# Kernel optimization log

Hardware: AMD Instinct MI355X
Metric: run time of the kernel (lower is better)

Reference implementation:

```python
import jax, jax.numpy as jnp
import numpy as np

B, T, F, H = 128, 1024, 256, 512  # batch, seq_len (input_dims[0]), features (input_dims[1]), rnn_size


def _lstm(xWb, U, reverse=False, return_sequences=False):
    """Keras-semantics LSTM. xWb: [B,T,4H] = x @ W + b precomputed. Gate order i,f,g,o."""
    Hn = U.shape[0]
    xs = jnp.swapaxes(xWb, 0, 1)  # [T,B,4H] for scan over time
    h0 = jnp.zeros((xWb.shape[0], Hn), xWb.dtype)
    c0 = h0

    def step(carry, xw):
        h, c = carry
        z = xw + h @ U  # [B,4H]
        i, f, g, o = jnp.split(z, 4, axis=-1)
        i = jax.nn.sigmoid(i)
        f = jax.nn.sigmoid(f)
        g = jnp.tanh(g)
        o = jax.nn.sigmoid(o)
        c = f * c + i * g
        h = o * jnp.tanh(c)
        return (h, c), h

    (hT, _), hs = jax.lax.scan(step, (h0, c0), xs, reverse=reverse)
    if return_sequences:
        return jnp.swapaxes(hs, 0, 1)  # [B,T,H]
    return hT  # [B,H] final state (for reverse=True this is the state after t=0)


def setup_inputs() -> dict:
    key = jax.random.key(0)
    ks = jax.random.split(key, 9)
    g = lambda k, shape: (jax.random.normal(k, shape, jnp.float32) * 0.05)
    return {
        "x": jax.random.uniform(ks[0], (B, T, F), jnp.float32),
        # encoder forward-direction LSTM
        "Wf": g(ks[1], (F, 4 * H)), "Uf": g(ks[2], (H, 4 * H)), "bf": jnp.zeros((4 * H,), jnp.float32),
        # encoder backward-direction LSTM
        "Wb": g(ks[3], (F, 4 * H)), "Ub": g(ks[4], (H, 4 * H)), "bb": jnp.zeros((4 * H,), jnp.float32),
        # decoder LSTM (input is concat latent, 2H wide)
        "Wd": g(ks[5], (2 * H, 4 * H)), "Ud": g(ks[6], (H, 4 * H)), "bd": jnp.zeros((4 * H,), jnp.float32),
        # TimeDistributed Dense
        "Wo": g(ks[7], (H, F)), "bo": jnp.zeros((F,), jnp.float32),
    }


def reference(x, Wf, Uf, bf, Wb, Ub, bb, Wd, Ud, bd, Wo, bo):
    # Encoder: Bidirectional(LSTM(H)) -> concat final states [B, 2H]
    h_fwd = _lstm(x @ Wf + bf, Uf, reverse=False)
    h_bwd = _lstm(x @ Wb + bb, Ub, reverse=True)
    latent = jnp.concatenate([h_fwd, h_bwd], axis=-1)  # [B, 2H]
    # Decoder: RepeatVector(T) -> LSTM(H, return_sequences) -> TimeDistributed(Dense(F))
    rep = jnp.broadcast_to(latent[:, None, :], (x.shape[0], x.shape[1], 2 * H))  # [B,T,2H]
    dec = _lstm(rep @ Wd + bd, Ud, return_sequences=True)  # [B,T,H]
    return dec @ Wo + bo  # [B,T,F]
```

## Files before the change

### kernel.cpp

```cpp
#include <hip/hip_runtime.h>
#include <stdint.h>

typedef unsigned short u16;
typedef short bf16x8 __attribute__((ext_vector_type(8)));
typedef float f32x4  __attribute__((ext_vector_type(4)));
typedef unsigned short u16x8 __attribute__((ext_vector_type(8)));
typedef unsigned int   u32x4 __attribute__((ext_vector_type(4)));

__device__ __forceinline__ u16 f2bf(float f) {
  uint32_t u = __float_as_uint(f);
  return (u16)((u + 0x7FFFu + ((u >> 16) & 1u)) >> 16);
}
__device__ __forceinline__ u16 f2bf6(float f) {
  uint32_t u = __float_as_uint(f);
  return (u16)(((u + 0xFFFFu + ((u >> 17) & 1u)) >> 17) << 1);
}
__device__ __forceinline__ float fsig(float x) {
  x = fminf(fmaxf(x, -30.f), 30.f);
  return __builtin_amdgcn_rcpf(1.f + __builtin_amdgcn_exp2f(-1.44269504088896f * x));
}
__device__ __forceinline__ float ftanhf(float x) {
  x = fminf(fmaxf(x, -10.f), 10.f);
  float e = __builtin_amdgcn_exp2f(2.88539008177793f * x);
  return (e - 1.f) * __builtin_amdgcn_rcpf(e + 1.f);
}

__device__ __forceinline__ int flag_load(const int* p) {
  int v;
  asm volatile("global_load_dword %0, %1, off sc0 sc1\n\ts_waitcnt vmcnt(0)"
               : "=&v"(v) : "v"(p) : "memory");
  return v;
}
__device__ __forceinline__ void flag_store(int* p, int v) {
  asm volatile("global_store_dword %0, %1, off sc0 sc1" :: "v"(p), "v"(v) : "memory");
}
__device__ __forceinline__ void ld_chunk4(const u16* p, u32x4& a, u32x4& b,
                                          u32x4& c, u32x4& d) {
  asm volatile("global_load_dwordx4 %0, %4, off sc0 sc1\n\t"
               "global_load_dwordx4 %1, %4, off offset:16 sc0 sc1\n\t"
               "global_load_dwordx4 %2, %4, off offset:32 sc0 sc1\n\t"
               "global_load_dwordx4 %3, %4, off offset:48 sc0 sc1\n\t"
               "s_waitcnt vmcnt(0)"
               : "=&v"(a), "=&v"(b), "=&v"(c), "=&v"(d)
               : "v"(p) : "memory");
}
__device__ __forceinline__ void st_coh_x4(u16* p, u32x4 v) {
  asm volatile("global_store_dwordx4 %0, %1, off sc0 sc1" :: "v"(p), "v"(v) : "memory");
}
__device__ __forceinline__ uint4 ld_x4(const float* p) {
  uint4 v;
  asm volatile("global_load_dwordx4 %0, %1, off" : "=&v"(v) : "v"(p) : "memory");
  return v;
}
__device__ __forceinline__ void wait_vm0() {
  asm volatile("s_waitcnt vmcnt(0)" ::: "memory");
}
__device__ __forceinline__ bf16x8 pin_frag(const u16* p) {
  u32x4 v;
  asm volatile("global_load_dwordx4 %0, %1, off" : "=&v"(v) : "v"(p));
  return __builtin_bit_cast(bf16x8, v);
}
__device__ __forceinline__ uint32_t nib_of(u32x4 d) {
  return (d[0] & 1u) | ((d[1] & 1u) << 1) | ((d[2] & 1u) << 2) | ((d[3] & 1u) << 3);
}

__global__ void prep_kernel(const float* __restrict__ Wf, const float* __restrict__ Uf, const float* __restrict__ bf,
                            const float* __restrict__ Wb, const float* __restrict__ Ub, const float* __restrict__ bb,
                            const float* __restrict__ Wd, const float* __restrict__ Ud, const float* __restrict__ bd,
                            const float* __restrict__ Wo,
                            u16* __restrict__ encF, u16* __restrict__ encB,
                            u16* __restrict__ udF, u16* __restrict__ wdF, u16* __restrict__ woF,
                            float* __restrict__ biasF, float* __restrict__ biasB, float* __restrict__ biasD,
                            int* __restrict__ flagsAll, u16* __restrict__ hbE, u16* __restrict__ hbD)
{
  constexpr int NC_ENC = 128 * 24 * 64;
  constexpr int NC_UD  = 128 * 16 * 64;
  constexpr int NC_WD  = 128 * 32 * 64;
  constexpr int NC_WO  = 16 * 16 * 64;
  constexpr int B1 = 2 * NC_ENC;
  constexpr int B2 = B1 + NC_UD;
  constexpr int B3 = B2 + NC_WD;
  constexpr int B4 = B3 + NC_WO;
  constexpr int B5 = B4 + 768;
  constexpr int B6 = B5 + 64;
  constexpr int B7 = B6 + 32768;
  constexpr int TOTAL = B7 + 16384;

  for (int idx = blockIdx.x * 256 + threadIdx.x; idx < TOTAL; idx += gridDim.x * 256) {
    if (idx < B1) {
      int d = idx / NC_ENC;
      int r = idx - d * NC_ENC;
      int ntg = r / 1536;
      int rem = r - ntg * 1536;
      int kt = rem >> 6, lane = rem & 63;
      int np = ntg * 16 + (lane & 15);
      int col = (np & 3) * 512 + (np >> 2);
      int kb = kt * 32 + (lane >> 4) * 8;
      const float* W = d ? Wb : Wf;
      const float* U = d ? Ub : Uf;
      u16* dst = (d ? encB : encF) + (size_t)r * 8;
      if (kb < 256) {
        const float* s = W + (size_t)kb * 2048 + col;
#pragma unroll
        for (int e = 0; e < 8; ++e) dst[e] = f2bf(s[(size_t)e * 2048]);
      } else {
        const float* s = U + (size_t)(kb - 256) * 2048 + col;
#pragma unroll
        for (int e = 0; e < 8; ++e) dst[e] = f2bf(s[(size_t)e * 2048]);
      }
    } else if (idx < B2) {
      int r = idx - B1;
      int ntg = r / 1024;
      int rem = r - ntg * 1024;
      int kt = rem >> 6, lane = rem & 63;
      int np = ntg * 16 + (lane & 15);
      int col = (np & 3) * 512 + (np >> 2);
      int kb = kt * 32 + (lane >> 4) * 8;
      const float* s = Ud + (size_t)kb * 2048 + col;
      u16* dst = udF + (size_t)r * 8;
#pragma unroll
      for (int e = 0; e < 8; ++e) dst[e] = f2bf(s[(size_t)e * 2048]);
    } else if (idx < B3) {
      int r = idx - B2;
      int ntg = r / 2048;
      int rem = r - ntg * 2048;
      int kt = rem >> 6, lane = rem & 63;
      int np = ntg * 16 + (lane & 15);
      int col = (np & 3) * 512 + (np >> 2);
      int kb = kt * 32 + (lane >> 4) * 8;
      const float* s = Wd + (size_t)kb * 2048 + col;
      u16* dst = wdF + (size_t)r * 8;
#pragma unroll
      for (int e = 0; e < 8; ++e) dst[e] = f2bf(s[(size_t)e * 2048]);
    } else if (idx < B4) {
      int r = idx - B3;
      int nt = r / 1024;
      int rem = r - nt * 1024;
      int kt = rem >> 6, lane = rem & 63;
      int col = nt * 16 + (lane & 15);
      int kb = kt * 32 + (lane >> 4) * 8;
      const float* s = Wo + (size_t)kb * 256 + col;
      u16* dst = woF + (size_t)r * 8;
#pragma unroll
      for (int e = 0; e < 8; ++e) dst[e] = f2bf(s[(size_t)e * 256]);
    } else if (idx < B5) {
      int r = idx - B4;
      int which = r >> 8;
      int j0 = (r & 255) * 8;
      const float* src = (which == 0) ? bf : (which == 1) ? bb : bd;
      float* dstb = (which == 0) ? biasF : (which == 1) ? biasB : biasD;
#pragma unroll
      for (int e = 0; e < 8; ++e) {
        int np = j0 + e;
        dstb[np] = src[(np & 3) * 512 + (np >> 2)];
      }
    } else if (idx < B6) {
      int r = idx - B5;
#pragma unroll
      for (int e = 0; e < 8; ++e) flagsAll[r * 8 + e] = 0;
    } else if (idx < B7) {
      int r = idx - B6;
      u16x8 z = {0, 0, 0, 0, 0, 0, 0, 0};
      *(u16x8*)&hbE[(size_t)r * 8] = z;
    } else {
      int r = idx - B7;
      u16x8 z = {0, 0, 0, 0, 0, 0, 0, 0};
      *(u16x8*)&hbD[(size_t)r * 8] = z;
    }
  }
}


__global__ __launch_bounds__(256, 1) void enc_kernel(
    const float* __restrict__ x,
    const u16* __restrict__ encF, const u16* __restrict__ encB,
    const float* __restrict__ biasF, const float* __restrict__ biasB,
    float* __restrict__ latent, u16* __restrict__ hbuf, int* __restrict__ flags)
{
  const int bid = blockIdx.x;
  const int g   = bid & 15;
  const int wgi = bid >> 4;
  const int dir = g >> 3;
  const int rowBase = (g & 7) * 16;
  const int tid = threadIdx.x;
  const int lane = tid & 63;
  const int wave = tid >> 6;
  const int l15 = lane & 15;
  const int lk  = lane >> 4;

  __shared__ __attribute__((aligned(16))) u16   xlds[2][16][264];
  __shared__ __attribute__((aligned(16))) u16   Alds[16][520];
  __shared__ __attribute__((aligned(16))) float zlds[4][2][16][20];
  __shared__ __attribute__((aligned(16))) u16   hlds[4][16][8];

  const u16* wsrc = dir ? encB : encF;
  bf16x8 Breg[2][24];
#pragma unroll
  for (int n = 0; n < 2; ++n) {
    const int ntg = wgi * 8 + wave * 2 + n;
    const u16* fb = wsrc + (size_t)(ntg * 1536 + lane) * 8;
#pragma unroll
    for (int kt = 0; kt < 24; ++kt)
      Breg[n][kt] = pin_frag(fb + kt * 512);
  }
  wait_vm0();
  __builtin_amdgcn_sched_barrier(0);

  const float* bias = dir ? biasB : biasF;
  float bias_r[2];
  bias_r[0] = bias[(wgi * 8 + wave * 2 + 0) * 16 + l15];
  bias_r[1] = bias[(wgi * 8 + wave * 2 + 1) * 16 + l15];

  u16* myH = hbuf + (size_t)g * 16384;
  int* myFlags = flags + g * 16;
  const int xr = tid >> 4, xc = tid & 15;
  const int cb = tid >> 2;
  const int cr0 = (tid & 3) * 4;

  {
    const int t0 = dir ? 1023 : 0;
    const float* xp = x + ((size_t)(rowBase + xr) * 1024 + t0) * 256 + xc * 16;
    float4 f0 = *(const float4*)xp;
    float4 f1 = *(const float4*)(xp + 4);
    float4 f2 = *(const float4*)(xp + 8);
    float4 f3 = *(const float4*)(xp + 12);
    u16x8 a, b;
    a[0]=f2bf(f0.x); a[1]=f2bf(f0.y); a[2]=f2bf(f0.z); a[3]=f2bf(f0.w);
    a[4]=f2bf(f1.x); a[5]=f2bf(f1.y); a[6]=f2bf(f1.z); a[7]=f2bf(f1.w);
    b[0]=f2bf(f2.x); b[1]=f2bf(f2.y); b[2]=f2bf(f2.z); b[3]=f2bf(f2.w);
    b[4]=f2bf(f3.x); b[5]=f2bf(f3.y); b[6]=f2bf(f3.z); b[7]=f2bf(f3.w);
    *(u16x8*)&xlds[0][xr][xc * 16] = a;
    *(u16x8*)&xlds[0][xr][xc * 16 + 8] = b;
  }
  __syncthreads();

  float cc0 = 0.f, cc1 = 0.f;

  for (int s = 0; s < 1024; ++s) {
    f32x4 acc0 = {bias_r[0], bias_r[0], bias_r[0], bias_r[0]};
    f32x4 acc1 = {bias_r[1], bias_r[1], bias_r[1], bias_r[1]};
#pragma unroll
    for (int kt = 0; kt < 8; ++kt) {
      bf16x8 av = *(const bf16x8*)&xlds[s & 1][l15][kt * 32 + lk * 8];
      acc0 = __builtin_amdgcn_mfma_f32_16x16x32_bf16(av, Breg[0][kt], acc0, 0, 0, 0);
      acc1 = __builtin_amdgcn_mfma_f32_16x16x32_bf16(av, Breg[1][kt], acc1, 0, 0, 0);
    }

    const int sn = (s + 1 < 1024) ? s + 1 : 1023;
    const int tn = dir ? (1023 - sn) : sn;
    const float* xp = x + ((size_t)(rowBase + xr) * 1024 + tn) * 256 + xc * 16;
    uint4 xq0 = ld_x4(xp);
    uint4 xq1 = ld_x4(xp + 4);
    uint4 xq2 = ld_x4(xp + 8);
    uint4 xq3 = ld_x4(xp + 12);

    if (s > 0) {
      const uint32_t Texp = 8u | ((uint32_t)s & 7u);
      const u16* hs = myH + ((s - 1) & 1) * 8192 + cb * 128 + cr0 * 8;
      const int* pf = &myFlags[tid >> 4];
      u32x4 h0, h1, h2, h3;
      int it = 0;
      while (true) {
        ld_chunk4(hs, h0, h1, h2, h3);
        if (nib_of(h0) == Texp && nib_of(h1) == Texp &&
            nib_of(h2) == Texp && nib_of(h3) == Texp) break;
        if ((it & 3) == 3 && flag_load(pf) >= s) {
          ld_chunk4(hs, h0, h1, h2, h3);
          break;
        }
        __builtin_amdgcn_s_sleep(1);
        if (++it > 200000) break;
      }
      h0 &= ~1u; h1 &= ~1u; h2 &= ~1u; h3 &= ~1u;
      *(u32x4*)&Alds[cr0][cb * 8]     = h0;
      *(u32x4*)&Alds[cr0 + 1][cb * 8] = h1;
      *(u32x4*)&Alds[cr0 + 2][cb * 8] = h2;
      *(u32x4*)&Alds[cr0 + 3][cb * 8] = h3;
      __syncthreads();
#pragma unroll
      for (int kt = 0; kt < 16; ++kt) {
        bf16x8 av = *(const bf16x8*)&Alds[l15][kt * 32 + lk * 8];
        acc0 = __builtin_amdgcn_mfma_f32_16x16x32_bf16(av, Breg[0][kt + 8], acc0, 0, 0, 0);
        acc1 = __builtin_amdgcn_mfma_f32_16x16x32_bf16(av, Breg[1][kt + 8], acc1, 0, 0, 0);
      }
    } else {
      wait_vm0();
      __builtin_amdgcn_sched_barrier(0);
    }

#pragma unroll
    for (int r = 0; r < 4; ++r) {
      zlds[wave][0][lk * 4 + r][l15] = acc0[r];
      zlds[wave][1][lk * 4 + r][l15] = acc1[r];
    }
    asm volatile("s_waitcnt lgkmcnt(0)" ::: "memory");
    float4 g0 = *(const float4*)&zlds[wave][0][l15][lk * 4];
    float4 g1 = *(const float4*)&zlds[wave][1][l15][lk * 4];
    float hv0, hv1;
    { float iv = fsig(g0.x), fv = fsig(g0.y), gg = ftanhf(g0.z), ov = fsig(g0.w);
      cc0 = fv * cc0 + iv * gg;  hv0 = ov * ftanhf(cc0); }
    { float iv = fsig(g1.x), fv = fsig(g1.y), gg = ftanhf(g1.z), ov = fsig(g1.w);
      cc1 = fv * cc1 + iv * gg;  hv1 = ov * ftanhf(cc1); }

    if (s < 1023) {
      const uint32_t T = 8u | ((uint32_t)(s + 1) & 7u);
      u16 v0, v1;
      if ((lk & 1) == 0) {
        uint32_t b0 = (lk == 0) ? (T & 1u) : ((T >> 1) & 1u);
        uint32_t b1 = (lk == 0) ? ((T >> 2) & 1u) : ((T >> 3) & 1u);
        v0 = f2bf6(hv0) | (u16)b0;
        v1 = f2bf6(hv1) | (u16)b1;
      } else {
        v0 = f2bf(hv0);
        v1 = f2bf(hv1);
      }
      hlds[wave][l15][lk]     = v0;
      hlds[wave][l15][lk + 4] = v1;
      asm volatile("s_waitcnt lgkmcnt(0)" ::: "memory");
      if (lane < 16) {
        const u32x4 c = *(const u32x4*)&hlds[wave][lane][0];
        u16* hw = myH + (s & 1) * 8192 + (wgi * 4 + wave) * 128 + lane * 8;
        st_coh_x4(hw, c);
      }
    } else {
      float* lp = latent + (size_t)(rowBase + l15) * 1024 + dir * 512 + wgi * 32 + wave * 8 + lk;
      lp[0] = hv0;
      lp[4] = hv1;
    }

    {
      float4 f0 = __builtin_bit_cast(float4, xq0);
      float4 f1 = __builtin_bit_cast(float4, xq1);
      float4 f2 = __builtin_bit_cast(float4, xq2);
      float4 f3 = __builtin_bit_cast(float4, xq3);
      u16x8 a, b;
      a[0]=f2bf(f0.x); a[1]=f2bf(f0.y); a[2]=f2bf(f0.z); a[3]=f2bf(f0.w);
      a[4]=f2bf(f1.x); a[5]=f2bf(f1.y); a[6]=f2bf(f1.z); a[7]=f2bf(f1.w);
      b[0]=f2bf(f2.x); b[1]=f2bf(f2.y); b[2]=f2bf(f2.z); b[3]=f2bf(f2.w);
      b[4]=f2bf(f3.x); b[5]=f2bf(f3.y); b[6]=f2bf(f3.z); b[7]=f2bf(f3.w);
      *(u16x8*)&xlds[(s + 1) & 1][xr][xc * 16] = a;
      *(u16x8*)&xlds[(s + 1) & 1][xr][xc * 16 + 8] = b;
    }

    wait_vm0();
    __syncthreads();
    if (tid == 0 && s < 1023) flag_store(&myFlags[wgi], s + 1);
  }
}

__global__ __launch_bounds__(256, 1) void dec_kernel(
    const float* __restrict__ latent,
    const u16* __restrict__ udF, const u16* __restrict__ wdF, const u16* __restrict__ woF,
    const float* __restrict__ biasD, const float* __restrict__ bo,
    float* __restrict__ out, u16* __restrict__ hbuf, int* __restrict__ flags)
{
  const int bid = blockIdx.x;
  const int g   = bid & 7;
  const int wgi = bid >> 3;
  const int rowBase = g * 16;
  const int tid = threadIdx.x;
  const int lane = tid & 63;
  const int wave = tid >> 6;
  const int l15 = lane & 15;
  const int lk  = lane >> 4;

  __shared__ __attribute__((aligned(16))) u16   Llds[16][1032];
  __shared__ __attribute__((aligned(16))) u16   Alds[2][16][520];
  __shared__ __attribute__((aligned(16))) float zlds[4][2][16][20];
  __shared__ __attribute__((aligned(16))) u16   hlds[4][16][8];

#pragma unroll
  for (int c8 = 0; c8 < 8; ++c8) {
    const int idx = tid + c8 * 256;
    const int rr = idx >> 7, cf = idx & 127;
    const float* lp = latent + (size_t)(rowBase + rr) * 1024 + cf * 8;
    float4 v0 = *(const float4*)lp;
    float4 v1 = *(const float4*)(lp + 4);
    u16x8 tv;
    tv[0]=f2bf(v0.x); tv[1]=f2bf(v0.y); tv[2]=f2bf(v0.z); tv[3]=f2bf(v0.w);
    tv[4]=f2bf(v1.x); tv[5]=f2bf(v1.y); tv[6]=f2bf(v1.z); tv[7]=f2bf(v1.w);
    *(u16x8*)&Llds[rr][cf * 8] = tv;
  }
  __syncthreads();

  f32x4 xwd[2];
#pragma unroll
  for (int n = 0; n < 2; ++n) {
    const int ntg = wgi * 8 + wave * 2 + n;
    const float br = biasD[ntg * 16 + l15];
    f32x4 xw = {br, br, br, br};
    const u16* wf = wdF + (size_t)(ntg * 2048 + lane) * 8;
#pragma unroll
    for (int kt = 0; kt < 32; ++kt) {
      bf16x8 b = *(const bf16x8*)(wf + kt * 512);
      bf16x8 a = *(const bf16x8*)&Llds[l15][kt * 32 + lk * 8];
      xw = __builtin_amdgcn_mfma_f32_16x16x32_bf16(a, b, xw, 0, 0, 0);
    }
    xwd[n] = xw;
  }

  bf16x8 Bu[2][16];
#pragma unroll
  for (int n = 0; n < 2; ++n) {
    const int ntg = wgi * 8 + wave * 2 + n;
    const u16* ub = udF + (size_t)(ntg * 1024 + lane) * 8;
#pragma unroll
    for (int kt = 0; kt < 16; ++kt)
      Bu[n][kt] = pin_frag(ub + kt * 512);
  }
  bf16x8 Bo[16];
  if (wave == 0) {
    const u16* ob = woF + (size_t)(wgi * 1024 + lane) * 8;
#pragma unroll
    for (int kt = 0; kt < 16; ++kt)
      Bo[kt] = pin_frag(ob + kt * 512);
  }
  wait_vm0();
  __builtin_amdgcn_sched_barrier(0);
  const float bo_r = bo[wgi * 16 + l15];

  u16* myH = hbuf + (size_t)g * 16384;
  int* myFlags = flags + g * 16;
  const int cb = tid >> 2;
  const int cr0 = (tid & 3) * 4;

  float cc0 = 0.f, cc1 = 0.f;

  for (int t = 0; t < 1024; ++t) {
    f32x4 acc0 = xwd[0], acc1 = xwd[1];

    if (t > 0) {
      const uint32_t Texp = 8u | ((uint32_t)t & 7u);
      const u16* hs = myH + ((t - 1) & 1) * 8192 + cb * 128 + cr0 * 8;
      const int* pf = &myFlags[tid >> 4];
      u32x4 h0, h1, h2, h3;
      int it = 0;
      while (true) {
        ld_chunk4(hs, h0, h1, h2, h3);
        if (nib_of(h0) == Texp && nib_of(h1) == Texp &&
            nib_of(h2) == Texp && nib_of(h3) == Texp) break;
        if ((it & 3) == 3 && flag_load(pf) >= t) {
          ld_chunk4(hs, h0, h1, h2, h3);
          break;
        }
        __builtin_amdgcn_s_sleep(1);
        if (++it > 200000) break;
      }
      h0 &= ~1u; h1 &= ~1u; h2 &= ~1u; h3 &= ~1u;
      *(u32x4*)&Alds[t & 1][cr0][cb * 8]     = h0;
      *(u32x4*)&Alds[t & 1][cr0 + 1][cb * 8] = h1;
      *(u32x4*)&Alds[t & 1][cr0 + 2][cb * 8] = h2;
      *(u32x4*)&Alds[t & 1][cr0 + 3][cb * 8] = h3;
      __syncthreads();
#pragma unroll
      for (int kt = 0; kt < 16; ++kt) {
        bf16x8 av = *(const bf16x8*)&Alds[t & 1][l15][kt * 32 + lk * 8];
        acc0 = __builtin_amdgcn_mfma_f32_16x16x32_bf16(av, Bu[0][kt], acc0, 0, 0, 0);
        acc1 = __builtin_amdgcn_mfma_f32_16x16x32_bf16(av, Bu[1][kt], acc1, 0, 0, 0);
      }
    }

#pragma unroll
    for (int r = 0; r < 4; ++r) {
      zlds[wave][0][lk * 4 + r][l15] = acc0[r];
      zlds[wave][1][lk * 4 + r][l15] = acc1[r];
    }
    asm volatile("s_waitcnt lgkmcnt(0)" ::: "memory");
    float4 g0 = *(const float4*)&zlds[wave][0][l15][lk * 4];
    float4 g1 = *(const float4*)&zlds[wave][1][l15][lk * 4];
    float hv0, hv1;
    { float iv = fsig(g0.x), fv = fsig(g0.y), gg = ftanhf(g0.z), ov = fsig(g0.w);
      cc0 = fv * cc0 + iv * gg;  hv0 = ov * ftanhf(cc0); }
    { float iv = fsig(g1.x), fv = fsig(g1.y), gg = ftanhf(g1.z), ov = fsig(g1.w);
      cc1 = fv * cc1 + iv * gg;  hv1 = ov * ftanhf(cc1); }

    {
      const uint32_t T = 8u | ((uint32_t)(t + 1) & 7u);
      u16 v0, v1;
      if ((lk & 1) == 0) {
        uint32_t b0 = (lk == 0) ? (T & 1u) : ((T >> 1) & 1u);
        uint32_t b1 = (lk == 0) ? ((T >> 2) & 1u) : ((T >> 3) & 1u);
        v0 = f2bf6(hv0) | (u16)b0;
        v1 = f2bf6(hv1) | (u16)b1;
      } else {
        v0 = f2bf(hv0);
        v1 = f2bf(hv1);
      }
      hlds[wave][l15][lk]     = v0;
      hlds[wave][l15][lk + 4] = v1;
      asm volatile("s_waitcnt lgkmcnt(0)" ::: "memory");
      if (lane < 16) {
        const u32x4 c = *(const u32x4*)&hlds[wave][lane][0];
        u16* hw = myH + (t & 1) * 8192 + (wgi * 4 + wave) * 128 + lane * 8;
        st_coh_x4(hw, c);
      }
      wait_vm0();
      __syncthreads();
      if (tid == 0) flag_store(&myFlags[wgi], t + 1);
    }

    if (t > 0 && wave == 0) {
      f32x4 od = {bo_r, bo_r, bo_r, bo_r};
#pragma unroll
      for (int kt = 0; kt < 16; ++kt) {
        bf16x8 a = *(const bf16x8*)&Alds[t & 1][l15][kt * 32 + lk * 8];
        od = __builtin_amdgcn_mfma_f32_16x16x32_bf16(a, Bo[kt], od, 0, 0, 0);
      }
#pragma unroll
      for (int r = 0; r < 4; ++r)
        out[((size_t)(rowBase + lk * 4 + r) * 1024 + (t - 1)) * 256 + wgi * 16 + l15] = od[r];
    }
  }

  {
    const uint32_t Texp = 8u;
    const u16* hs = myH + 8192 + cb * 128 + cr0 * 8;
    const int* pf = &myFlags[tid >> 4];
    u32x4 h0, h1, h2, h3;
    int it = 0;
    while (true) {
      ld_chunk4(hs, h0, h1, h2, h3);
      if (nib_of(h0) == Texp && nib_of(h1) == Texp &&
          nib_of(h2) == Texp && nib_of(h3) == Texp) break;
      if ((it & 3) == 3 && flag_load(pf) >= 1024) {
        ld_chunk4(hs, h0, h1, h2, h3);
        break;
      }
      __builtin_amdgcn_s_sleep(1);
      if (++it > 200000) break;
    }
    h0 &= ~1u; h1 &= ~1u; h2 &= ~1u; h3 &= ~1u;
    *(u32x4*)&Alds[0][cr0][cb * 8]     = h0;
    *(u32x4*)&Alds[0][cr0 + 1][cb * 8] = h1;
    *(u32x4*)&Alds[0][cr0 + 2][cb * 8] = h2;
    *(u32x4*)&Alds[0][cr0 + 3][cb * 8] = h3;
    __syncthreads();
    if (wave == 0) {
      f32x4 od = {bo_r, bo_r, bo_r, bo_r};
#pragma unroll
      for (int kt = 0; kt < 16; ++kt) {
        bf16x8 a = *(const bf16x8*)&Alds[0][l15][kt * 32 + lk * 8];
        od = __builtin_amdgcn_mfma_f32_16x16x32_bf16(a, Bo[kt], od, 0, 0, 0);
      }
#pragma unroll
      for (int r = 0; r < 4; ++r)
        out[((size_t)(rowBase + lk * 4 + r) * 1024 + 1023) * 256 + wgi * 16 + l15] = od[r];
    }
  }
}

extern "C" void kernel_launch(void* const* d_in, const int* in_sizes, int n_in,
                              void* d_out, int out_size, void* d_ws, size_t ws_size,
                              hipStream_t stream)
{
  const float* x  = (const float*)d_in[0];
  const float* Wf = (const float*)d_in[1];
  const float* Uf = (const float*)d_in[2];
  const float* bf = (const float*)d_in[3];
  const float* Wb = (const float*)d_in[4];
  const float* Ub = (const float*)d_in[5];
  const float* bb = (const float*)d_in[6];
  const float* Wd = (const float*)d_in[7];
  const float* Ud = (const float*)d_in[8];
  const float* bd = (const float*)d_in[9];
  const float* Wo = (const float*)d_in[10];
  const float* bo = (const float*)d_in[11];

  if (ws_size < 14182400) return;

  char* ws = (char*)d_ws;
  u16*  encF   = (u16*)(ws + 0);
  u16*  encB   = (u16*)(ws + 3145728);
  u16*  udF    = (u16*)(ws + 6291456);
  u16*  wdF    = (u16*)(ws + 8388608);
  u16*  woF    = (u16*)(ws + 12582912);
  float* biasF = (float*)(ws + 12845056);
  float* biasB = (float*)(ws + 12853248);
  float* biasD = (float*)(ws + 12861440);
  float* latent= (float*)(ws + 12869632);
  u16*  hbufE  = (u16*)(ws + 13393920);
  u16*  hbufD  = (u16*)(ws + 13918208);
  int*  flagsE = (int*)(ws + 14180352);
  int*  flagsD = (int*)(ws + 14181376);

  prep_kernel<<<256, 256, 0, stream>>>(Wf, Uf, bf, Wb, Ub, bb, Wd, Ud, bd, Wo,
                                       encF, encB, udF, wdF, woF,
                                       biasF, biasB, biasD, flagsE, hbufE, hbufD);
  enc_kernel<<<256, 256, 0, stream>>>(x, encF, encB, biasF, biasB, latent, hbufE, flagsE);
  dec_kernel<<<128, 256, 0, stream>>>(latent, udF, wdF, woF, biasD, bo,
                                      (float*)d_out, hbufD, flagsD);
}
```

Baseline: 4.731 ms.

## Drop flag-based fallback sync and double-buffer recurrent h tile in LDS

Removes the per-step flag store/load handshake (and the wait_vm0 + extra barrier before it) from both encoder and decoder, relying solely on the tag bits embedded in the bf16 h values for cross-workgroup readiness. The encoder's recurrent A tile is now double-buffered in LDS so the h-load, x conversion and a single __syncthreads are merged before the recurrent MFMAs, eliminating one barrier per step. This shortens the serial per-timestep critical path, but it gives up the fallback path: if tagged stores become visible only partially, readers spin until the larger timeout.

```diff
diff --git a/kernel.cpp b/kernel.cpp
--- a/kernel.cpp
+++ b/kernel.cpp
@@ -25,15 +25,6 @@
   return (e - 1.f) * __builtin_amdgcn_rcpf(e + 1.f);
 }
 
-__device__ __forceinline__ int flag_load(const int* p) {
-  int v;
-  asm volatile("global_load_dword %0, %1, off sc0 sc1\n\ts_waitcnt vmcnt(0)"
-               : "=&v"(v) : "v"(p) : "memory");
-  return v;
-}
-__device__ __forceinline__ void flag_store(int* p, int v) {
-  asm volatile("global_store_dword %0, %1, off sc0 sc1" :: "v"(p), "v"(v) : "memory");
-}
 __device__ __forceinline__ void ld_chunk4(const u16* p, u32x4& a, u32x4& b,
                                           u32x4& c, u32x4& d) {
   asm volatile("global_load_dwordx4 %0, %4, off sc0 sc1\n\t"
@@ -175,7 +166,7 @@
     const float* __restrict__ x,
     const u16* __restrict__ encF, const u16* __restrict__ encB,
     const float* __restrict__ biasF, const float* __restrict__ biasB,
-    float* __restrict__ latent, u16* __restrict__ hbuf, int* __restrict__ flags)
+    float* __restrict__ latent, u16* __restrict__ hbuf)
 {
   const int bid = blockIdx.x;
   const int g   = bid & 15;
@@ -189,7 +180,7 @@
   const int lk  = lane >> 4;
 
   __shared__ __attribute__((aligned(16))) u16   xlds[2][16][264];
-  __shared__ __attribute__((aligned(16))) u16   Alds[16][520];
+  __shared__ __attribute__((aligned(16))) u16   Alds[2][16][520];
   __shared__ __attribute__((aligned(16))) float zlds[4][2][16][20];
   __shared__ __attribute__((aligned(16))) u16   hlds[4][16][8];
 
@@ -212,7 +203,6 @@
   bias_r[1] = bias[(wgi * 8 + wave * 2 + 1) * 16 + l15];
 
   u16* myH = hbuf + (size_t)g * 16384;
-  int* myFlags = flags + g * 16;
   const int xr = tid >> 4, xc = tid & 15;
   const int cb = tid >> 2;
   const int cr0 = (tid & 3) * 4;
@@ -257,77 +247,24 @@
     if (s > 0) {
       const uint32_t Texp = 8u | ((uint32_t)s & 7u);
       const u16* hs = myH + ((s - 1) & 1) * 8192 + cb * 128 + cr0 * 8;
-      const int* pf = &myFlags[tid >> 4];
       u32x4 h0, h1, h2, h3;
       int it = 0;
       while (true) {
         ld_chunk4(hs, h0, h1, h2, h3);
         if (nib_of(h0) == Texp && nib_of(h1) == Texp &&
             nib_of(h2) == Texp && nib_of(h3) == Texp) break;
-        if ((it & 3) == 3 && flag_load(pf) >= s) {
-          ld_chunk4(hs, h0, h1, h2, h3);
-          break;
-        }
         __builtin_amdgcn_s_sleep(1);
-        if (++it > 200000) break;
+        if (++it > 400000) break;
       }
       h0 &= ~1u; h1 &= ~1u; h2 &= ~1u; h3 &= ~1u;
-      *(u32x4*)&Alds[cr0][cb * 8]     = h0;
-      *(u32x4*)&Alds[cr0 + 1][cb * 8] = h1;
-      *(u32x4*)&Alds[cr0 + 2][cb * 8] = h2;
-      *(u32x4*)&Alds[cr0 + 3][cb * 8] = h3;
-      __syncthreads();
-#pragma unroll
-      for (int kt = 0; kt < 16; ++kt) {
-        bf16x8 av = *(const bf16x8*)&Alds[l15][kt * 32 + lk * 8];
-        acc0 = __builtin_amdgcn_mfma_f32_16x16x32_bf16(av, Breg[0][kt + 8], acc0, 0, 0, 0);
-        acc1 = __builtin_amdgcn_mfma_f32_16x16x32_bf16(av, Breg[1][kt + 8], acc1, 0, 0, 0);
-      }
+      *(u32x4*)&Alds[s & 1][cr0][cb * 8]     = h0;
+      *(u32x4*)&Alds[s & 1][cr0 + 1][cb * 8] = h1;
+      *(u32x4*)&Alds[s & 1][cr0 + 2][cb * 8] = h2;
+      *(u32x4*)&Alds[s & 1][cr0 + 3][cb * 8] = h3;
     } else {
       wait_vm0();
       __builtin_amdgcn_sched_barrier(0);
     }
-
-#pragma unroll
-    for (int r = 0; r < 4; ++r) {
-      zlds[wave][0][lk * 4 + r][l15] = acc0[r];
-      zlds[wave][1][lk * 4 + r][l15] = acc1[r];
-    }
-    asm volatile("s_waitcnt lgkmcnt(0)" ::: "memory");
-    float4 g0 = *(const float4*)&zlds[wave][0][l15][lk * 4];
-    float4 g1 = *(const float4*)&zlds[wave][1][l15][lk * 4];
-    float hv0, hv1;
-    { float iv = fsig(g0.x), fv = fsig(g0.y), gg = ftanhf(g0.z), ov = fsig(g0.w);
-      cc0 = fv * cc0 + iv * gg;  hv0 = ov * ftanhf(cc0); }
-    { float iv = fsig(g1.x), fv = fsig(g1.y), gg = ftanhf(g1.z), ov = fsig(g1.w);
-      cc1 = fv * cc1 + iv * gg;  hv1 = ov * ftanhf(cc1); }
-
-    if (s < 1023) {
-      const uint32_t T = 8u | ((uint32_t)(s + 1) & 7u);
-      u16 v0, v1;
-      if ((lk & 1) == 0) {
-        uint32_t b0 = (lk == 0) ? (T & 1u) : ((T >> 1) & 1u);
-        uint32_t b1 = (lk == 0) ? ((T >> 2) & 1u) : ((T >> 3) & 1u);
-        v0 = f2bf6(hv0) | (u16)b0;
-        v1 = f2bf6(hv1) | (u16)b1;
-      } else {
-        v0 = f2bf(hv0);
-        v1 = f2bf(hv1);
-      }
-      hlds[wave][l15][lk]     = v0;
-      hlds[wave][l15][lk + 4] = v1;
-      asm volatile("s_waitcnt lgkmcnt(0)" ::: "memory");
-      if (lane < 16) {
-        const u32x4 c = *(const u32x4*)&hlds[wave][lane][0];
-        u16* hw = myH + (s & 1) * 8192 + (wgi * 4 + wave) * 128 + lane * 8;
-        st_coh_x4(hw, c);
-      }
-    } else {
-      float* lp = latent + (size_t)(rowBase + l15) * 1024 + dir * 512 + wgi * 32 + wave * 8 + lk;
-      lp[0] = hv0;
-      lp[4] = hv1;
-    }
-
     {
       float4 f0 = __builtin_bit_cast(float4, xq0);
       float4 f1 = __builtin_bit_cast(float4, xq1);
@@ -341,10 +278,56 @@
       *(u16x8*)&xlds[(s + 1) & 1][xr][xc * 16] = a;
       *(u16x8*)&xlds[(s + 1) & 1][xr][xc * 16 + 8] = b;
     }
-
-    wait_vm0();
     __syncthreads();
-    if (tid == 0 && s < 1023) flag_store(&myFlags[wgi], s + 1);
+
+    if (s > 0) {
+#pragma unroll
+      for (int kt = 0; kt < 16; ++kt) {
+        bf16x8 av = *(const bf16x8*)&Alds[s & 1][l15][kt * 32 + lk * 8];
+        acc0 = __builtin_amdgcn_mfma_f32_16x16x32_bf16(av, Breg[0][kt + 8], acc0, 0, 0, 0);
+        acc1 = __builtin_amdgcn_mfma_f32_16x16x32_bf16(av, Breg[1][kt + 8], acc1, 0, 0, 0);
+      }
+    }
+
+#pragma unroll
+    for (int r = 0; r < 4; ++r) {
+      zlds[wave][0][lk * 4 + r][l15] = acc0[r];
+      zlds[wave][1][lk * 4 + r][l15] = acc1[r];
+    }
+    asm volatile("s_waitcnt lgkmcnt(0)" ::: "memory");
+    float4 g0 = *(const float4*)&zlds[wave][0][l15][lk * 4];
+    float4 g1 = *(const float4*)&zlds[wave][1][l15][lk * 4];
+    float hv0, hv1;
+    { float iv = fsig(g0.x), fv = fsig(g0.y), gg = ftanhf(g0.z), ov = fsig(g0.w);
+      cc0 = fv * cc0 + iv * gg;  hv0 = ov * ftanhf(cc0); }
+    { float iv = fsig(g1.x), fv = fsig(g1.y), gg = ftanhf(g1.z), ov = fsig(g1.w);
+      cc1 = fv * cc1 + iv * gg;  hv1 = ov * ftanhf(cc1); }
+
+    if (s < 1023) {
+      const uint32_t T = 8u | ((uint32_t)(s + 1) & 7u);
+      u16 v0, v1;
+      if ((lk & 1) == 0) {
+        uint32_t b0 = (lk == 0) ? (T & 1u) : ((T >> 1) & 1u);
+        uint32_t b1 = (lk == 0) ? ((T >> 2) & 1u) : ((T >> 3) & 1u);
+        v0 = f2bf6(hv0) | (u16)b0;
+        v1 = f2bf6(hv1) | (u16)b1;
+      } else {
+        v0 = f2bf(hv0);
+        v1 = f2bf(hv1);
+      }
+      hlds[wave][l15][lk]     = v0;
+      hlds[wave][l15][lk + 4] = v1;
+      asm volatile("s_waitcnt lgkmcnt(0)" ::: "memory");
+      if (lane < 16) {
+        const u32x4 c = *(const u32x4*)&hlds[wave][lane][0];
+        u16* hw = myH + (s & 1) * 8192 + (wgi * 4 + wave) * 128 + lane * 8;
+        st_coh_x4(hw, c);
+      }
+    } else {
+      float* lp = latent + (size_t)(rowBase + l15) * 1024 + dir * 512 + wgi * 32 + wave * 8 + lk;
+      lp[0] = hv0;
+      lp[4] = hv1;
+    }
   }
 }
 
@@ -352,7 +335,7 @@
     const float* __restrict__ latent,
     const u16* __restrict__ udF, const u16* __restrict__ wdF, const u16* __restrict__ woF,
     const float* __restrict__ biasD, const float* __restrict__ bo,
-    float* __restrict__ out, u16* __restrict__ hbuf, int* __restrict__ flags)
+    float* __restrict__ out, u16* __restrict__ hbuf)
 {
   const int bid = blockIdx.x;
   const int g   = bid & 7;
@@ -420,7 +403,6 @@
   const float bo_r = bo[wgi * 16 + l15];
 
   u16* myH = hbuf + (size_t)g * 16384;
-  int* myFlags = flags + g * 16;
   const int cb = tid >> 2;
   const int cr0 = (tid & 3) * 4;
 
@@ -432,19 +414,14 @@
     if (t > 0) {
       const uint32_t Texp = 8u | ((uint32_t)t & 7u);
       const u16* hs = myH + ((t - 1) & 1) * 8192 + cb * 128 + cr0 * 8;
-      const int* pf = &myFlags[tid >> 4];
       u32x4 h0, h1, h2, h3;
       int it = 0;
       while (true) {
         ld_chunk4(hs, h0, h1, h2, h3);
         if (nib_of(h0) == Texp && nib_of(h1) == Texp &&
             nib_of(h2) == Texp && nib_of(h3) == Texp) break;
-        if ((it & 3) == 3 && flag_load(pf) >= t) {
-          ld_chunk4(hs, h0, h1, h2, h3);
-          break;
-        }
         __builtin_amdgcn_s_sleep(1);
-        if (++it > 200000) break;
+        if (++it > 400000) break;
       }
       h0 &= ~1u; h1 &= ~1u; h2 &= ~1u; h3 &= ~1u;
       *(u32x4*)&Alds[t & 1][cr0][cb * 8]     = h0;
@@ -494,9 +471,6 @@
         u16* hw = myH + (t & 1) * 8192 + (wgi * 4 + wave) * 128 + lane * 8;
         st_coh_x4(hw, c);
       }
-      wait_vm0();
-      __syncthreads();
-      if (tid == 0) flag_store(&myFlags[wgi], t + 1);
     }
 
     if (t > 0 && wave == 0) {
@@ -515,19 +489,14 @@
   {
     const uint32_t Texp = 8u;
     const u16* hs = myH + 8192 + cb * 128 + cr0 * 8;
-    const int* pf = &myFlags[tid >> 4];
     u32x4 h0, h1, h2, h3;
     int it = 0;
     while (true) {
       ld_chunk4(hs, h0, h1, h2, h3);
       if (nib_of(h0) == Texp && nib_of(h1) == Texp &&
           nib_of(h2) == Texp && nib_of(h3) == Texp) break;
-      if ((it & 3) == 3 && flag_load(pf) >= 1024) {
-        ld_chunk4(hs, h0, h1, h2, h3);
-        break;
-      }
       __builtin_amdgcn_s_sleep(1);
-      if (++it > 200000) break;
+      if (++it > 400000) break;
     }
     h0 &= ~1u; h1 &= ~1u; h2 &= ~1u; h3 &= ~1u;
     *(u32x4*)&Alds[0][cr0][cb * 8]     = h0;
@@ -581,12 +550,11 @@
   u16*  hbufE  = (u16*)(ws + 13393920);
   u16*  hbufD  = (u16*)(ws + 13918208);
   int*  flagsE = (int*)(ws + 14180352);
-  int*  flagsD = (int*)(ws + 14181376);
 
   prep_kernel<<<256, 256, 0, stream>>>(Wf, Uf, bf, Wb, Ub, bb, Wd, Ud, bd, Wo,
                                        encF, encB, udF, wdF, woF,
                                        biasF, biasB, biasD, flagsE, hbufE, hbufD);
-  enc_kernel<<<256, 256, 0, stream>>>(x, encF, encB, biasF, biasB, latent, hbufE, flagsE);
+  enc_kernel<<<256, 256, 0, stream>>>(x, encF, encB, biasF, biasB, latent, hbufE);
   dec_kernel<<<128, 256, 0, stream>>>(latent, udF, wdF, woF, biasD, bo,
-                                      (float*)d_out, hbufD, flagsD);
-}
+                                      (float*)d_out, hbufD);
+}
```

Result: no change. 4.720 ms, median of 2 (-0.2%).
